# Kernel optimization log

Hardware: AMD Instinct MI355X
Metric: run time of the kernel (lower is better)

The kernel has to match this reference:

```python
import jax, jax.numpy as jnp
import numpy as np
import math

EPS = 1e-3          # self.eps
M = 0.5             # margin
H = 0.333           # rad_h
S = 64.0            # scale
HEAD_B = 0.5        # head_b
BATCH_MEAN = 0.0    # registered buffer initial value
BATCH_STD = 100.0   # registered buffer initial value
B, D, C = 1024, 512, 51332


def setup_inputs() -> dict:
    key = jax.random.key(0)
    k1, k2, k3, k4 = jax.random.split(key, 4)
    emb = jax.random.normal(k1, (B, D), dtype=jnp.float32)
    # face embeddings are typically l2-normalized before this head
    emb = emb / jnp.clip(jnp.linalg.norm(emb, axis=1, keepdims=True), 1e-5)
    # feature norms in a realistic range [5, 35)
    norms = jax.random.uniform(k2, (B, 1), dtype=jnp.float32) * 30.0 + 5.0
    kernel = jax.random.normal(k3, (D, C), dtype=jnp.float32)
    label = jax.random.randint(k4, (B,), 0, C)
    return {"embbedings": emb, "norms": norms, "kernel": kernel, "label": label}


def reference(embbedings, norms, kernel, label):
    # l2_norm(kernel, axis=0)
    kn = kernel / jnp.clip(jnp.linalg.norm(kernel, axis=0, keepdims=True), 1e-5)
    # [B, C] cosine logits
    cosine = jnp.clip(embbedings @ kn, -1.0 + EPS, 1.0 - EPS)
    # detached norm-based margin scaler ('batchnorm' branch)
    safe_norms = jax.lax.stop_gradient(jnp.clip(norms, 1e-3, 100.0))
    ms = jnp.clip((safe_norms - BATCH_MEAN) / (BATCH_STD + EPS) * H, -1.0, 1.0)[:, 0]  # [B]
    rows = jnp.arange(cosine.shape[0])
    # additive angular margin only at the label column (equivalent to the one-hot scatter)
    theta = jnp.arccos(cosine).at[rows, label].add(M * ms)
    cos_m = jnp.cos(jnp.clip(theta, EPS, math.pi - EPS))
    # subtractive cosine margin at the label column
    cos_m = cos_m.at[rows, label].add(-(HEAD_B - M * ms))
    return cos_m * S
```

## Files before the change

### kernel.cpp

```cpp
#include <hip/hip_runtime.h>
#include <hip/hip_bf16.h>
#include <math.h>

#define B_ROWS 1024
#define DDIM   512
#define CN     51332
#define CPAD   51456
#define EPSF   1e-3f
#define SCALE  64.0f
#define NT     8

typedef unsigned short ushort_t;
typedef short bf16x8 __attribute__((ext_vector_type(8)));
typedef float f32x4  __attribute__((ext_vector_type(4)));
typedef unsigned short us8 __attribute__((ext_vector_type(8)));
typedef unsigned short us4 __attribute__((ext_vector_type(4)));

static __device__ __forceinline__ unsigned short f2bf(float f) {
    unsigned int u = __float_as_uint(f);
    u += 0x7fffu + ((u >> 16) & 1u);
    return (unsigned short)(u >> 16);
}

__global__ void colpass(const float* __restrict__ kern, ushort_t* __restrict__ kbT,
                        float* __restrict__ partials) {
    const int c2 = (blockIdx.x * 256 + threadIdx.x) * 2;
    if (c2 >= CPAD) return;
    const int d0 = blockIdx.y * 64;
    const bool valid = (c2 < CN);
    float s0 = 0.f, s1 = 0.f;
    for (int d = d0; d < d0 + 64; d += 8) {
        us8 p0, p1;
#pragma unroll
        for (int j = 0; j < 8; ++j) {
            float x = 0.f, y = 0.f;
            if (valid) {
                const float2 v = *(const float2*)&kern[(size_t)(d + j) * CN + c2];
                x = v.x; y = v.y;
            }
            s0 += x * x; s1 += y * y;
            p0[j] = f2bf(x); p1[j] = f2bf(y);
        }
        *(us8*)&kbT[(size_t)c2 * DDIM + d]       = p0;
        *(us8*)&kbT[(size_t)(c2 + 1) * DDIM + d] = p1;
    }
    partials[(size_t)blockIdx.y * CPAD + c2]     = s0;
    partials[(size_t)blockIdx.y * CPAD + c2 + 1] = s1;
}

__global__ void finnorm(const float* __restrict__ partials, float* __restrict__ inv_norm) {
    const int c = blockIdx.x * 256 + threadIdx.x;
    float s = 0.f;
#pragma unroll
    for (int k = 0; k < 8; ++k) s += partials[(size_t)k * CPAD + c];
    inv_norm[c] = 1.0f / fmaxf(sqrtf(s), 1e-5f);
}

__global__ void embcast(const float* __restrict__ emb, ushort_t* __restrict__ embb) {
    const int t = blockIdx.x * 256 + threadIdx.x;
    const float4 v = ((const float4*)emb)[t];
    us4 o; o[0] = f2bf(v.x); o[1] = f2bf(v.y); o[2] = f2bf(v.z); o[3] = f2bf(v.w);
    *(us4*)&embb[(size_t)t * 4] = o;
}

#define MFMA(d, va, vb) (d) = __builtin_amdgcn_mfma_f32_16x16x32_bf16((va), (vb), (d), 0, 0, 0)

#define STAGE16(gp, lp) __builtin_amdgcn_global_load_lds( \
    (__attribute__((address_space(1))) void*)(gp), \
    (__attribute__((address_space(3))) void*)(lp), 16, 0, 0)

#define STAGE(gl, sb, half, kstep) do { \
    const int rb_ = (half) * 128 + w * 16; \
    STAGE16((gl) + (size_t)rb_ * DDIM + (size_t)(kstep) * 64, &(sb)[rb_ * 64]); \
    STAGE16((gl) + (size_t)(rb_ + 8) * DDIM + (size_t)(kstep) * 64, &(sb)[(rb_ + 8) * 64]); \
} while (0)

__global__ __launch_bounds__(512, 2) void gemm_kernel(
        const ushort_t* __restrict__ embb, const ushort_t* __restrict__ kbT,
        const float* __restrict__ inv_norm, float* __restrict__ out) {
    __shared__ ushort_t smem[65536];

    const int tid  = threadIdx.x;
    const int lane = tid & 63;
    const int w    = tid >> 6;
    const int wm = w >> 2, wn = w & 3;
    const int lm = lane & 15, lq = lane >> 4;
    const int r8 = lane >> 3, c8 = lane & 7;

    const int bid = blockIdx.x;
    const int xcd = bid & 7, loc = bid >> 3;
    const int u  = (xcd < 4) ? (xcd * 101 + loc) : (404 + (xcd - 4) * 100 + loc);
    const int m0 = (u & 3) * 256;
    const int n0 = (u >> 2) * 256;

    const ushort_t* gAl = embb + (size_t)(m0 + r8) * DDIM + ((c8 ^ r8) << 3);
    const ushort_t* gBl = kbT  + (size_t)(n0 + r8) * DDIM + ((c8 ^ r8) << 3);
    const int swz = lm & 7;
    const int ca0 = ((lq    ) ^ swz) << 3;
    const int ca1 = ((lq + 4) ^ swz) << 3;
    const int offA = (wm * 128 + lm) * 64;
    const int offB = (wn * 64  + lm) * 64;

    f32x4 acc[8][4];
#pragma unroll
    for (int i = 0; i < 8; ++i)
#pragma unroll
        for (int j = 0; j < 4; ++j) acc[i][j] = (f32x4){0.f, 0.f, 0.f, 0.f};

    STAGE(gAl, (smem        ), 0, 0); STAGE(gAl, (smem        ), 1, 0);
    STAGE(gBl, (smem + 32768), 0, 0); STAGE(gBl, (smem + 32768), 1, 0);
    STAGE(gAl, (smem + 16384), 0, 1); STAGE(gAl, (smem + 16384), 1, 1);
    STAGE(gBl, (smem + 49152), 0, 1);
    asm volatile("s_waitcnt vmcnt(6)" ::: "memory");
    __builtin_amdgcn_s_barrier();
    __builtin_amdgcn_sched_barrier(0);

    bf16x8 a[8][2], b0[2][2], b1[2][2];

    for (int t = 0; t < NT; ++t) {
        const int cur = t & 1;
        ushort_t* Sa = smem + cur * 16384;
        ushort_t* Sb = smem + 32768 + cur * 16384;
        ushort_t* Nb = smem + 32768 + (cur ^ 1) * 16384;
        const int kA = (t + 2) & 7;
        const int kB = (t + 1) & 7;

#pragma unroll
        for (int i = 0; i < 8; ++i) {
            a[i][0] = *(const bf16x8*)&Sa[offA + i * 1024 + ca0];
            a[i][1] = *(const bf16x8*)&Sa[offA + i * 1024 + ca1];
        }
#pragma unroll
        for (int j = 0; j < 2; ++j) {
            b0[j][0] = *(const bf16x8*)&Sb[offB + j * 1024 + ca0];
            b0[j][1] = *(const bf16x8*)&Sb[offB + j * 1024 + ca1];
        }
        STAGE(gBl, Nb, 1, kB);
        __builtin_amdgcn_s_barrier();
        __builtin_amdgcn_s_setprio(1);
#pragma unroll
        for (int i = 0; i < 4; ++i)
#pragma unroll
            for (int j = 0; j < 2; ++j) {
                MFMA(acc[i][j], a[i][0], b0[j][0]);
                MFMA(acc[i][j], a[i][1], b0[j][1]);
            }
        __builtin_amdgcn_s_setprio(0);
        __builtin_amdgcn_s_barrier();
        __builtin_amdgcn_sched_barrier(0);

#pragma unroll
        for (int j = 0; j < 2; ++j) {
            b1[j][0] = *(const bf16x8*)&Sb[offB + (j + 2) * 1024 + ca0];
            b1[j][1] = *(const bf16x8*)&Sb[offB + (j + 2) * 1024 + ca1];
        }
        STAGE(gAl, Sa, 0, kA);
        __builtin_amdgcn_s_barrier();
        __builtin_amdgcn_s_setprio(1);
#pragma unroll
        for (int i = 0; i < 4; ++i)
#pragma unroll
            for (int j = 0; j < 2; ++j) {
                MFMA(acc[i][j + 2], a[i][0], b1[j][0]);
                MFMA(acc[i][j + 2], a[i][1], b1[j][1]);
            }
        __builtin_amdgcn_s_setprio(0);
        __builtin_amdgcn_s_barrier();
        __builtin_amdgcn_sched_barrier(0);

        STAGE(gAl, Sa, 1, kA);
        __builtin_amdgcn_s_barrier();
        __builtin_amdgcn_s_setprio(1);
#pragma unroll
        for (int i = 4; i < 8; ++i)
#pragma unroll
            for (int j = 0; j < 2; ++j) {
                MFMA(acc[i][j], a[i][0], b0[j][0]);
                MFMA(acc[i][j], a[i][1], b0[j][1]);
            }
        __builtin_amdgcn_s_setprio(0);
        __builtin_amdgcn_s_barrier();
        __builtin_amdgcn_sched_barrier(0);

        STAGE(gBl, Sb, 0, kA);
        __builtin_amdgcn_s_barrier();
        __builtin_amdgcn_s_setprio(1);
#pragma unroll
        for (int i = 4; i < 8; ++i)
#pragma unroll
            for (int j = 0; j < 2; ++j) {
                MFMA(acc[i][j + 2], a[i][0], b1[j][0]);
                MFMA(acc[i][j + 2], a[i][1], b1[j][1]);
            }
        __builtin_amdgcn_s_setprio(0);
        asm volatile("s_waitcnt vmcnt(6)" ::: "memory");
        __builtin_amdgcn_s_barrier();
        __builtin_amdgcn_sched_barrier(0);
    }

    asm volatile("s_waitcnt vmcnt(0)" ::: "memory");
    __syncthreads();

    float invn[4];
#pragma unroll
    for (int j = 0; j < 4; ++j) {
        const int col = n0 + wn * 64 + j * 16 + lm;
        invn[j] = (col < CN) ? inv_norm[col] : 0.f;
    }
    float* Ew = (float*)smem + w * 1024;
    const int rr = lane >> 4, cc = lane & 15;
#pragma unroll
    for (int i = 0; i < 8; ++i) {
#pragma unroll
        for (int j = 0; j < 4; ++j)
#pragma unroll
            for (int r = 0; r < 4; ++r) {
                const int row = lq * 4 + r;
                const int cs  = ((j * 16 + lm) + row * 4) & 63;
                float v = acc[i][j][r] * invn[j];
                v = fminf(fmaxf(v, -(1.0f - EPSF)), 1.0f - EPSF) * SCALE;
                Ew[row * 64 + cs] = v;
            }
#pragma unroll
        for (int rep = 0; rep < 4; ++rep) {
            const int row = rep * 4 + rr;
            const f32x4 v = *(const f32x4*)&Ew[row * 64 + ((cc + row) & 15) * 4];
            const int grow = m0 + wm * 128 + i * 16 + row;
            const int gcol = n0 + wn * 64 + cc * 4;
            if (gcol < CN)
                *(f32x4*)&out[(size_t)grow * CN + gcol] = v;
        }
    }
}

__global__ void fixup(const float* __restrict__ norms, const int* __restrict__ label,
                      float* __restrict__ out) {
    const int b = blockIdx.x * 256 + threadIdx.x;
    if (b >= B_ROWS) return;
    const int c = label[b];
    const float safe = fminf(fmaxf(norms[b], 1e-3f), 100.0f);
    const float ms = fminf(fmaxf(safe / (100.0f + 1e-3f) * 0.333f, -1.0f), 1.0f);
    const size_t idx = (size_t)b * CN + c;
    const float cosv = out[idx] * (1.0f / SCALE);
    float theta = acosf(cosv) + 0.5f * ms;
    theta = fminf(fmaxf(theta, EPSF), 3.14159265358979f - EPSF);
    out[idx] = (cosf(theta) - (0.5f - 0.5f * ms)) * SCALE;
}

extern "C" void kernel_launch(void* const* d_in, const int* in_sizes, int n_in,
                              void* d_out, int out_size, void* d_ws, size_t ws_size,
                              hipStream_t stream) {
    const float* emb   = (const float*)d_in[0];
    const float* norms = (const float*)d_in[1];
    const float* kern  = (const float*)d_in[2];
    const int*   label = (const int*)d_in[3];
    float* out = (float*)d_out;

    char* ws = (char*)d_ws;
    ushort_t* kbT = (ushort_t*)ws;
    size_t off = (size_t)CPAD * DDIM * 2;
    ushort_t* embb = (ushort_t*)(ws + off); off += (size_t)B_ROWS * DDIM * 2;
    float* inv_norm = (float*)(ws + off);   off += (size_t)CPAD * 4;
    float* partials = (float*)(ws + off);

    colpass<<<dim3((CPAD / 2 + 255) / 256, 8), 256, 0, stream>>>(kern, kbT, partials);
    embcast<<<dim3((B_ROWS * DDIM / 4) / 256), 256, 0, stream>>>(emb, embb);
    finnorm<<<dim3(CPAD / 256), 256, 0, stream>>>(partials, inv_norm);
    gemm_kernel<<<dim3(804), 512, 0, stream>>>(embb, kbT, inv_norm, out);
    fixup<<<dim3(B_ROWS / 256), 256, 0, stream>>>(norms, label, out);
}
```

Baseline: 431.1 us.

## Shrink GEMM tile to 256x128 and widen colpass to four columns per thread

The GEMM block tile is halved in N from 256x256 to 256x128. Each warp now computes a 64x64 sub-tile, the grid doubles to 1608 blocks, and the pipeline shrinks to two MFMA phases per k-step with smaller LDS. Separately, the kernel-transpose/cast pass now loads float4 per thread across 16 rows before packing to bf16, to raise memory-level parallelism. The change trades operand reuse per block for more blocks and lower LDS/register pressure. It also adds a redundant extra block to the fixup launch.

```diff
diff --git a/kernel.cpp b/kernel.cpp
--- a/kernel.cpp
+++ b/kernel.cpp
@@ -24,28 +24,35 @@
 
 __global__ void colpass(const float* __restrict__ kern, ushort_t* __restrict__ kbT,
                         float* __restrict__ partials) {
-    const int c2 = (blockIdx.x * 256 + threadIdx.x) * 2;
-    if (c2 >= CPAD) return;
+    const int c4 = (blockIdx.x * 256 + threadIdx.x) * 4;
+    if (c4 >= CPAD) return;
     const int d0 = blockIdx.y * 64;
-    const bool valid = (c2 < CN);
-    float s0 = 0.f, s1 = 0.f;
-    for (int d = d0; d < d0 + 64; d += 8) {
-        us8 p0, p1;
-#pragma unroll
-        for (int j = 0; j < 8; ++j) {
-            float x = 0.f, y = 0.f;
-            if (valid) {
-                const float2 v = *(const float2*)&kern[(size_t)(d + j) * CN + c2];
-                x = v.x; y = v.y;
-            }
-            s0 += x * x; s1 += y * y;
-            p0[j] = f2bf(x); p1[j] = f2bf(y);
-        }
-        *(us8*)&kbT[(size_t)c2 * DDIM + d]       = p0;
-        *(us8*)&kbT[(size_t)(c2 + 1) * DDIM + d] = p1;
-    }
-    partials[(size_t)blockIdx.y * CPAD + c2]     = s0;
-    partials[(size_t)blockIdx.y * CPAD + c2 + 1] = s1;
+    const bool valid = (c4 < CN);
+    float s0 = 0.f, s1 = 0.f, s2 = 0.f, s3 = 0.f;
+#pragma unroll
+    for (int g = 0; g < 4; ++g) {
+        float4 v[16];
+#pragma unroll
+        for (int j = 0; j < 16; ++j)
+            v[j] = valid ? *(const float4*)&kern[(size_t)(d0 + g * 16 + j) * CN + c4]
+                         : make_float4(0.f, 0.f, 0.f, 0.f);
+        us8 p[4][2];
+#pragma unroll
+        for (int j = 0; j < 16; ++j) {
+            s0 += v[j].x * v[j].x; s1 += v[j].y * v[j].y;
+            s2 += v[j].z * v[j].z; s3 += v[j].w * v[j].w;
+            p[0][j >> 3][j & 7] = f2bf(v[j].x);
+            p[1][j >> 3][j & 7] = f2bf(v[j].y);
+            p[2][j >> 3][j & 7] = f2bf(v[j].z);
+            p[3][j >> 3][j & 7] = f2bf(v[j].w);
+        }
+#pragma unroll
+        for (int cc = 0; cc < 4; ++cc) {
+            *(us8*)&kbT[(size_t)(c4 + cc) * DDIM + d0 + g * 16]     = p[cc][0];
+            *(us8*)&kbT[(size_t)(c4 + cc) * DDIM + d0 + g * 16 + 8] = p[cc][1];
+        }
+    }
+    *(float4*)&partials[(size_t)blockIdx.y * CPAD + c4] = make_float4(s0, s1, s2, s3);
 }
 
 __global__ void finnorm(const float* __restrict__ partials, float* __restrict__ inv_norm) {
@@ -78,55 +85,58 @@
 __global__ __launch_bounds__(512, 2) void gemm_kernel(
         const ushort_t* __restrict__ embb, const ushort_t* __restrict__ kbT,
         const float* __restrict__ inv_norm, float* __restrict__ out) {
-    __shared__ ushort_t smem[65536];
+    __shared__ ushort_t smem[49152];
 
     const int tid  = threadIdx.x;
     const int lane = tid & 63;
     const int w    = tid >> 6;
-    const int wm = w >> 2, wn = w & 3;
+    const int wm = w >> 1, wn = w & 1;
     const int lm = lane & 15, lq = lane >> 4;
     const int r8 = lane >> 3, c8 = lane & 7;
 
     const int bid = blockIdx.x;
-    const int xcd = bid & 7, loc = bid >> 3;
-    const int u  = (xcd < 4) ? (xcd * 101 + loc) : (404 + (xcd - 4) * 100 + loc);
-    const int m0 = (u & 3) * 256;
-    const int n0 = (u >> 2) * 256;
+    const int u   = (bid & 7) * 201 + (bid >> 3);
+    const int m0  = (u & 3) * 256;
+    const int n0  = (u >> 2) * 128;
 
     const ushort_t* gAl = embb + (size_t)(m0 + r8) * DDIM + ((c8 ^ r8) << 3);
     const ushort_t* gBl = kbT  + (size_t)(n0 + r8) * DDIM + ((c8 ^ r8) << 3);
     const int swz = lm & 7;
     const int ca0 = ((lq    ) ^ swz) << 3;
     const int ca1 = ((lq + 4) ^ swz) << 3;
-    const int offA = (wm * 128 + lm) * 64;
-    const int offB = (wn * 64  + lm) * 64;
-
-    f32x4 acc[8][4];
-#pragma unroll
-    for (int i = 0; i < 8; ++i)
+    const int offA = (wm * 64 + lm) * 64;
+    const int offB = (wn * 64 + lm) * 64;
+
+    f32x4 acc[4][4];
+#pragma unroll
+    for (int i = 0; i < 4; ++i)
 #pragma unroll
         for (int j = 0; j < 4; ++j) acc[i][j] = (f32x4){0.f, 0.f, 0.f, 0.f};
 
-    STAGE(gAl, (smem        ), 0, 0); STAGE(gAl, (smem        ), 1, 0);
-    STAGE(gBl, (smem + 32768), 0, 0); STAGE(gBl, (smem + 32768), 1, 0);
-    STAGE(gAl, (smem + 16384), 0, 1); STAGE(gAl, (smem + 16384), 1, 1);
-    STAGE(gBl, (smem + 49152), 0, 1);
-    asm volatile("s_waitcnt vmcnt(6)" ::: "memory");
+    ushort_t* A0 = smem;
+    ushort_t* A1 = smem + 16384;
+    ushort_t* B0 = smem + 32768;
+    ushort_t* B1 = smem + 40960;
+
+    STAGE(gAl, A0, 0, 0); STAGE(gAl, A0, 1, 0);
+    STAGE(gBl, B0, 0, 0);
+    STAGE(gAl, A1, 0, 1); STAGE(gAl, A1, 1, 1);
+    asm volatile("s_waitcnt vmcnt(4)" ::: "memory");
     __builtin_amdgcn_s_barrier();
     __builtin_amdgcn_sched_barrier(0);
 
-    bf16x8 a[8][2], b0[2][2], b1[2][2];
+    bf16x8 a[4][2], b0[2][2], b1[2][2];
 
     for (int t = 0; t < NT; ++t) {
         const int cur = t & 1;
-        ushort_t* Sa = smem + cur * 16384;
-        ushort_t* Sb = smem + 32768 + cur * 16384;
-        ushort_t* Nb = smem + 32768 + (cur ^ 1) * 16384;
+        ushort_t* Sa  = (cur == 0) ? A0 : A1;
+        ushort_t* Sb  = (cur == 0) ? B0 : B1;
+        ushort_t* SbN = (cur == 0) ? B1 : B0;
         const int kA = (t + 2) & 7;
         const int kB = (t + 1) & 7;
 
 #pragma unroll
-        for (int i = 0; i < 8; ++i) {
+        for (int i = 0; i < 4; ++i) {
             a[i][0] = *(const bf16x8*)&Sa[offA + i * 1024 + ca0];
             a[i][1] = *(const bf16x8*)&Sa[offA + i * 1024 + ca1];
         }
@@ -135,7 +145,7 @@
             b0[j][0] = *(const bf16x8*)&Sb[offB + j * 1024 + ca0];
             b0[j][1] = *(const bf16x8*)&Sb[offB + j * 1024 + ca1];
         }
-        STAGE(gBl, Nb, 1, kB);
+        STAGE(gBl, SbN, 0, kB);
         __builtin_amdgcn_s_barrier();
         __builtin_amdgcn_s_setprio(1);
 #pragma unroll
@@ -154,7 +164,7 @@
             b1[j][0] = *(const bf16x8*)&Sb[offB + (j + 2) * 1024 + ca0];
             b1[j][1] = *(const bf16x8*)&Sb[offB + (j + 2) * 1024 + ca1];
         }
-        STAGE(gAl, Sa, 0, kA);
+        STAGE(gAl, Sa, 0, kA); STAGE(gAl, Sa, 1, kA);
         __builtin_amdgcn_s_barrier();
         __builtin_amdgcn_s_setprio(1);
 #pragma unroll
@@ -165,35 +175,7 @@
                 MFMA(acc[i][j + 2], a[i][1], b1[j][1]);
             }
         __builtin_amdgcn_s_setprio(0);
-        __builtin_amdgcn_s_barrier();
-        __builtin_amdgcn_sched_barrier(0);
-
-        STAGE(gAl, Sa, 1, kA);
-        __builtin_amdgcn_s_barrier();
-        __builtin_amdgcn_s_setprio(1);
-#pragma unroll
-        for (int i = 4; i < 8; ++i)
-#pragma unroll
-            for (int j = 0; j < 2; ++j) {
-                MFMA(acc[i][j], a[i][0], b0[j][0]);
-                MFMA(acc[i][j], a[i][1], b0[j][1]);
-            }
-        __builtin_amdgcn_s_setprio(0);
-        __builtin_amdgcn_s_barrier();
-        __builtin_amdgcn_sched_barrier(0);
-
-        STAGE(gBl, Sb, 0, kA);
-        __builtin_amdgcn_s_barrier();
-        __builtin_amdgcn_s_setprio(1);
-#pragma unroll
-        for (int i = 4; i < 8; ++i)
-#pragma unroll
-            for (int j = 0; j < 2; ++j) {
-                MFMA(acc[i][j + 2], a[i][0], b1[j][0]);
-                MFMA(acc[i][j + 2], a[i][1], b1[j][1]);
-            }
-        __builtin_amdgcn_s_setprio(0);
-        asm volatile("s_waitcnt vmcnt(6)" ::: "memory");
+        asm volatile("s_waitcnt vmcnt(4)" ::: "memory");
         __builtin_amdgcn_s_barrier();
         __builtin_amdgcn_sched_barrier(0);
     }
@@ -210,7 +192,7 @@
     float* Ew = (float*)smem + w * 1024;
     const int rr = lane >> 4, cc = lane & 15;
 #pragma unroll
-    for (int i = 0; i < 8; ++i) {
+    for (int i = 0; i < 4; ++i) {
 #pragma unroll
         for (int j = 0; j < 4; ++j)
 #pragma unroll
@@ -225,7 +207,7 @@
         for (int rep = 0; rep < 4; ++rep) {
             const int row = rep * 4 + rr;
             const f32x4 v = *(const f32x4*)&Ew[row * 64 + ((cc + row) & 15) * 4];
-            const int grow = m0 + wm * 128 + i * 16 + row;
+            const int grow = m0 + wm * 64 + i * 16 + row;
             const int gcol = n0 + wn * 64 + cc * 4;
             if (gcol < CN)
                 *(f32x4*)&out[(size_t)grow * CN + gcol] = v;
@@ -263,9 +245,9 @@
     float* inv_norm = (float*)(ws + off);   off += (size_t)CPAD * 4;
     float* partials = (float*)(ws + off);
 
-    colpass<<<dim3((CPAD / 2 + 255) / 256, 8), 256, 0, stream>>>(kern, kbT, partials);
+    colpass<<<dim3((CPAD / 4 + 255) / 256, 8), 256, 0, stream>>>(kern, kbT, partials);
     embcast<<<dim3((B_ROWS * DDIM / 4) / 256), 256, 0, stream>>>(emb, embb);
     finnorm<<<dim3(CPAD / 256), 256, 0, stream>>>(partials, inv_norm);
-    gemm_kernel<<<dim3(804), 512, 0, stream>>>(embb, kbT, inv_norm, out);
-    fixup<<<dim3(B_ROWS / 256), 256, 0, stream>>>(norms, label, out);
-}
+    gemm_kernel<<<dim3(1608), 512, 0, stream>>>(embb, kbT, inv_norm, out);
+    fixup<<<dim3(B_ROWS / 256 + 1), 256, 0, stream>>>(norms, label, out);
+}
```

Measured after the change: 494.4 us. 14.7% more time.
